# Optimization experiments

Measured on AMD Instinct MI355X. Metric: run time of the kernel, lower is better.

## Reference

```python
import jax, jax.numpy as jnp
import numpy as np

N_NODES = 100000
N_EDGES = 1600000
IN_DIM = 128
HID = 128
OUT = 112


def setup_inputs() -> dict:
    key = jax.random.key(0)
    ks = jax.random.split(key, 8)
    s = 1.0 / np.sqrt(IN_DIM)
    sh = 1.0 / np.sqrt(HID)
    return {
        "x": jax.random.normal(ks[0], (N_NODES, IN_DIM), jnp.float32),
        "edge_index": jax.random.randint(ks[1], (2, N_EDGES), 0, N_NODES, jnp.int64),
        "W_l1": jax.random.normal(ks[2], (HID, IN_DIM), jnp.float32) * s,
        "b_l1": jnp.zeros((HID,), jnp.float32),
        "W_r1": jax.random.normal(ks[3], (HID, IN_DIM), jnp.float32) * s,
        "W_l2": jax.random.normal(ks[4], (HID, HID), jnp.float32) * sh,
        "b_l2": jnp.zeros((HID,), jnp.float32),
        "W_r2": jax.random.normal(ks[5], (HID, HID), jnp.float32) * sh,
        "W_out": jax.random.normal(ks[6], (OUT, HID), jnp.float32) * sh,
        "b_out": jnp.zeros((OUT,), jnp.float32),
    }


def _sage_conv(x, edge_index, W_l, b_l, W_r):
    # PyG SAGEConv, aggr='mean', root_weight=True:
    #   out_i = W_l @ mean_{j in N(i)} x_j + b_l + W_r @ x_i
    src, dst = edge_index[0], edge_index[1]
    n = x.shape[0]
    agg = jax.ops.segment_sum(x[src], dst, num_segments=n)          # [N, d]
    deg = jax.ops.segment_sum(jnp.ones_like(dst, dtype=x.dtype), dst, num_segments=n)
    mean = agg / jnp.maximum(deg, 1.0)[:, None]
    return mean @ W_l.T + b_l + x @ W_r.T


def reference(x, edge_index, W_l1, b_l1, W_r1, W_l2, b_l2, W_r2, W_out, b_out):
    h = jax.nn.relu(_sage_conv(x, edge_index, W_l1, b_l1, W_r1))
    # dropout p=0.2 is identity at inference (training=False)
    h = jax.nn.relu(_sage_conv(h, edge_index, W_l2, b_l2, W_r2))
    return h @ W_out.T + b_out  # [N, 112] logits
```

## Files before the change

### kernel.cpp

```cpp
#include <hip/hip_runtime.h>
#include <hip/hip_bf16.h>

#define HID 128
#define OUT_DIM 112
#define CAP 4096

typedef short bf16x8 __attribute__((ext_vector_type(8)));
typedef float f32x4 __attribute__((ext_vector_type(4)));

__device__ __forceinline__ ushort f2b(float f) {
  __hip_bfloat16 h = __float2bfloat16(f);
  return *reinterpret_cast<ushort*>(&h);
}

__global__ __launch_bounds__(256) void f2b_kernel(
    const float* __restrict__ in, ushort* __restrict__ out, int n4) {
  int i = blockIdx.x * 256 + threadIdx.x;
  if (i >= n4) return;
  float4 v = ((const float4*)in)[i];
  ushort4 r;
  r.x = f2b(v.x); r.y = f2b(v.y); r.z = f2b(v.z); r.w = f2b(v.w);
  ((ushort4*)out)[i] = r;
}

__global__ __launch_bounds__(256) void packw_kernel(
    const float* __restrict__ W, ushort* __restrict__ wb, int ntiles, int total) {
  int p = blockIdx.x * 256 + threadIdx.x;
  if (p >= total) return;
  int j = p & 7;
  int l = (p >> 3) & 63;
  int rest = p >> 9;
  int nt = rest % ntiles;
  int ks = rest / ntiles;
  int nn = nt * 16 + (l & 15);
  int k = ks * 32 + (l >> 4) * 8 + j;
  wb[p] = f2b(W[nn * 128 + k]);
}

__global__ __launch_bounds__(256) void hist_kernel(
    const int* __restrict__ dst, int* __restrict__ gcount, int e, int nb) {
  __shared__ int lh[1024];
  const int t = threadIdx.x;
  for (int i = t; i < nb; i += 256) lh[i] = 0;
  __syncthreads();
  int base = blockIdx.x * 4096;
#pragma unroll
  for (int j = 0; j < 16; ++j) {
    int i = base + j * 256 + t;
    if (i < e) atomicAdd(&lh[dst[i] >> 7], 1);
  }
  __syncthreads();
  for (int i = t; i < nb; i += 256)
    if (lh[i]) atomicAdd(&gcount[i], lh[i]);
}

__global__ __launch_bounds__(1024) void scan_nb_kernel(
    const int* __restrict__ gcount, int* __restrict__ gbase,
    int* __restrict__ gcursor, int* __restrict__ rowstart,
    int e, int n, int nb) {
  __shared__ int wsum[16];
  const int t = threadIdx.x, lane = t & 63, wid = t >> 6;
  int v = (t < nb) ? gcount[t] : 0;
  int s = v;
#pragma unroll
  for (int off = 1; off < 64; off <<= 1) {
    int u = __shfl_up(s, off, 64);
    if (lane >= off) s += u;
  }
  if (lane == 63) wsum[wid] = s;
  __syncthreads();
  if (wid == 0) {
    int ws = (lane < 16) ? wsum[lane] : 0;
#pragma unroll
    for (int off = 1; off < 16; off <<= 1) {
      int u = __shfl_up(ws, off, 64);
      if (lane >= off) ws += u;
    }
    if (lane < 16) wsum[lane] = ws;
  }
  __syncthreads();
  int excl = s - v + (wid ? wsum[wid - 1] : 0);
  if (t < nb) {
    gbase[t] = excl;
    gcursor[t] = excl;
  }
  if (t == 0) {
    gbase[nb] = e;
    rowstart[n] = e;
  }
}

__global__ __launch_bounds__(1024) void bucket_scatter_kernel(
    const int* __restrict__ src, const int* __restrict__ dst,
    int* __restrict__ gcursor, uint* __restrict__ bedges, int e, int nb) {
  __shared__ int lh[1024];
  __shared__ int lstart[1024];
  __shared__ int wsum[16];
  __shared__ uint sp[8192];
  __shared__ ushort sb[8192];
  const int t = threadIdx.x, lane = t & 63, wid = t >> 6;
  const int base = blockIdx.x * 8192;
  const int ecnt = min(8192, e - base);
  for (int i = t; i < nb; i += 1024) lh[i] = 0;
  __syncthreads();
  int myb[8], myr[8];
  uint myp[8];
#pragma unroll
  for (int j = 0; j < 8; ++j) {
    int i = base + j * 1024 + t;
    myb[j] = -1;
    if (i < e) {
      int d = dst[i];
      int sv = src[i];
      int b = d >> 7;
      myb[j] = b;
      myp[j] = ((uint)sv << 7) | (uint)(d & 127);
      myr[j] = atomicAdd(&lh[b], 1);
    }
  }
  __syncthreads();
  int cnt = (t < nb) ? lh[t] : 0;
  int s = cnt;
#pragma unroll
  for (int off = 1; off < 64; off <<= 1) {
    int u = __shfl_up(s, off, 64);
    if (lane >= off) s += u;
  }
  if (lane == 63) wsum[wid] = s;
  __syncthreads();
  if (wid == 0) {
    int ws = (lane < 16) ? wsum[lane] : 0;
#pragma unroll
    for (int off = 1; off < 16; off <<= 1) {
      int u = __shfl_up(ws, off, 64);
      if (lane >= off) ws += u;
    }
    if (lane < 16) wsum[lane] = ws;
  }
  __syncthreads();
  int excl = s - cnt + (wid ? wsum[wid - 1] : 0);
  if (t < nb) lstart[t] = excl;
  __syncthreads();
  if (t < nb) lh[t] = (cnt > 0) ? atomicAdd(&gcursor[t], cnt) : 0;
  __syncthreads();
#pragma unroll
  for (int j = 0; j < 8; ++j) {
    if (myb[j] >= 0) {
      int slot = lstart[myb[j]] + myr[j];
      sp[slot] = myp[j];
      sb[slot] = (ushort)myb[j];
    }
  }
  __syncthreads();
#pragma unroll
  for (int j = 0; j < 8; ++j) {
    int i = j * 1024 + t;
    if (i < ecnt) {
      int b = sb[i];
      int pos = lh[b] + (i - lstart[b]);
      bedges[pos] = sp[i];
    }
  }
}

__global__ __launch_bounds__(256) void csr_build_kernel(
    const uint* __restrict__ bedges, const int* __restrict__ gbase,
    int* __restrict__ rowstart, float* __restrict__ dinv,
    int* __restrict__ csr_src, int n) {
  __shared__ int lh[128];
  __shared__ int lst[128];
  __shared__ int lcur[128];
  __shared__ int wsum2[4];
  __shared__ int lsorted[CAP];
  const int t = threadIdx.x;
  const int bkt = blockIdx.x;
  const int node0 = bkt << 7;
  const int g0 = gbase[bkt], g1 = gbase[bkt + 1];
  const int cnt = g1 - g0;
  if (t < 128) lh[t] = 0;
  __syncthreads();
  for (int i = t; i < cnt; i += 256)
    atomicAdd(&lh[bedges[g0 + i] & 127], 1);
  __syncthreads();
  const int lane = t & 63, wid = t >> 6;
  int v = (t < 128) ? lh[t] : 0;
  int s = v;
#pragma unroll
  for (int off = 1; off < 64; off <<= 1) {
    int u = __shfl_up(s, off, 64);
    if (lane >= off) s += u;
  }
  if (t < 128 && lane == 63) wsum2[wid] = s;
  __syncthreads();
  int excl = s - v + ((wid == 1) ? wsum2[0] : 0);
  if (t < 128) {
    lst[t] = excl;
    lcur[t] = excl;
    int node = node0 + t;
    if (node < n) {
      rowstart[node] = g0 + excl;
      dinv[node] = 1.0f / (float)max(v, 1);
    }
  }
  __syncthreads();
  for (int i = t; i < cnt; i += 256) {
    uint p = bedges[g0 + i];
    int d = p & 127;
    int slot = atomicAdd(&lcur[d], 1);
    int sv = (int)(p >> 7);
    if (slot < CAP) lsorted[slot] = sv;
    else csr_src[g0 + slot] = sv;
  }
  __syncthreads();
  int lim = min(cnt, CAP);
  for (int i = t; i < lim; i += 256) csr_src[g0 + i] = lsorted[i];
}

__global__ __launch_bounds__(256) void agg_bf16_kernel(
    const ushort* __restrict__ xb, const int* __restrict__ csr_src,
    const int* __restrict__ rowstart, const float* __restrict__ dinv,
    ushort* __restrict__ aggb, int n) {
  int node = blockIdx.x * 4 + (threadIdx.x >> 6);
  int lane = threadIdx.x & 63;
  if (node >= n) return;
  int s = rowstart[node], e1 = rowstart[node + 1];
  float ax = 0.f, ay = 0.f;
  int e = s;
  for (; e + 4 <= e1; e += 4) {
    int s0 = csr_src[e], s1 = csr_src[e + 1], s2 = csr_src[e + 2], s3 = csr_src[e + 3];
    uint u0 = ((const uint*)(xb + (size_t)s0 * 128))[lane];
    uint u1 = ((const uint*)(xb + (size_t)s1 * 128))[lane];
    uint u2 = ((const uint*)(xb + (size_t)s2 * 128))[lane];
    uint u3 = ((const uint*)(xb + (size_t)s3 * 128))[lane];
    ax += (__uint_as_float(u0 << 16) + __uint_as_float(u1 << 16)) +
          (__uint_as_float(u2 << 16) + __uint_as_float(u3 << 16));
    ay += (__uint_as_float(u0 & 0xffff0000u) + __uint_as_float(u1 & 0xffff0000u)) +
          (__uint_as_float(u2 & 0xffff0000u) + __uint_as_float(u3 & 0xffff0000u));
  }
  for (; e < e1; ++e) {
    uint u = ((const uint*)(xb + (size_t)csr_src[e] * 128))[lane];
    ax += __uint_as_float(u << 16);
    ay += __uint_as_float(u & 0xffff0000u);
  }
  float sc = dinv[node];
  uint r = (uint)f2b(ax * sc) | ((uint)f2b(ay * sc) << 16);
  ((uint*)(aggb + (size_t)node * 128))[lane] = r;
}

__global__ __launch_bounds__(256) void lin_mfma_kernel(
    const ushort* __restrict__ meanb, const ushort* __restrict__ xb,
    const ushort* __restrict__ wb, const float* __restrict__ bias,
    ushort* __restrict__ outb, int n) {
  __shared__ ushort zA[64 * 128];
  __shared__ ushort zX[64 * 128];
  const int t = threadIdx.x;
  const int block0 = blockIdx.x * 64;
#pragma unroll
  for (int i = 0; i < 4; ++i) {
    int c = i * 256 + t;
    int row = c >> 4;
    int col = c & 15;
    int node = block0 + row;
    int4 va = make_int4(0, 0, 0, 0), vx = make_int4(0, 0, 0, 0);
    if (node < n) {
      va = ((const int4*)(meanb + (size_t)node * 128))[col];
      vx = ((const int4*)(xb + (size_t)node * 128))[col];
    }
    ((int4*)zA)[c] = va;
    ((int4*)zX)[c] = vx;
  }
  __syncthreads();
  const int lane = t & 63;
  const int wave = t >> 6;
  const int m0 = wave * 16;
  const int cidx = lane & 15;
  const int quad = lane >> 4;
  f32x4 acc[8];
#pragma unroll
  for (int nt = 0; nt < 8; ++nt) acc[nt] = (f32x4){0.f, 0.f, 0.f, 0.f};
#pragma unroll
  for (int s = 0; s < 2; ++s) {
    const ushort* zs = (s == 0) ? zA : zX;
#pragma unroll
    for (int ks = 0; ks < 4; ++ks) {
      bf16x8 a = *(const bf16x8*)(zs + (m0 + cidx) * 128 + ks * 32 + quad * 8);
      const ushort* wp = wb + ((size_t)((s * 4 + ks) * 8) * 64 + lane) * 8;
#pragma unroll
      for (int nt = 0; nt < 8; ++nt) {
        bf16x8 b = *(const bf16x8*)(wp + nt * 512);
        acc[nt] = __builtin_amdgcn_mfma_f32_16x16x32_bf16(a, b, acc[nt], 0, 0, 0);
      }
    }
  }
  __syncthreads();
#pragma unroll
  for (int nt = 0; nt < 8; ++nt) {
    float bv = bias[nt * 16 + cidx];
#pragma unroll
    for (int i = 0; i < 4; ++i) {
      float v = fmaxf(acc[nt][i] + bv, 0.f);
      zA[(m0 + quad * 4 + i) * 128 + nt * 16 + cidx] = f2b(v);
    }
  }
  __syncthreads();
#pragma unroll
  for (int i = 0; i < 4; ++i) {
    int c = i * 256 + t;
    int row = c >> 4;
    int col = c & 15;
    int node = block0 + row;
    if (node < n) ((int4*)(outb + (size_t)node * 128))[col] = ((const int4*)zA)[c];
  }
}

__global__ __launch_bounds__(256) void out_mfma_kernel(
    const ushort* __restrict__ h2b, const ushort* __restrict__ wb,
    const float* __restrict__ bias, float* __restrict__ outp, int n) {
  __shared__ ushort zt[64 * 128];
  __shared__ float zo[64 * 112];
  const int t = threadIdx.x;
  const int block0 = blockIdx.x * 64;
#pragma unroll
  for (int i = 0; i < 4; ++i) {
    int c = i * 256 + t;
    int row = c >> 4;
    int col = c & 15;
    int node = block0 + row;
    int4 v = make_int4(0, 0, 0, 0);
    if (node < n) v = ((const int4*)(h2b + (size_t)node * 128))[col];
    ((int4*)zt)[c] = v;
  }
  __syncthreads();
  const int lane = t & 63;
  const int wave = t >> 6;
  const int m0 = wave * 16;
  const int cidx = lane & 15;
  const int quad = lane >> 4;
  f32x4 acc[7];
#pragma unroll
  for (int nt = 0; nt < 7; ++nt) acc[nt] = (f32x4){0.f, 0.f, 0.f, 0.f};
#pragma unroll
  for (int ks = 0; ks < 4; ++ks) {
    bf16x8 a = *(const bf16x8*)(zt + (m0 + cidx) * 128 + ks * 32 + quad * 8);
    const ushort* wp = wb + ((size_t)(ks * 7) * 64 + lane) * 8;
#pragma unroll
    for (int nt = 0; nt < 7; ++nt) {
      bf16x8 b = *(const bf16x8*)(wp + nt * 512);
      acc[nt] = __builtin_amdgcn_mfma_f32_16x16x32_bf16(a, b, acc[nt], 0, 0, 0);
    }
  }
#pragma unroll
  for (int nt = 0; nt < 7; ++nt) {
    float bv = bias[nt * 16 + cidx];
#pragma unroll
    for (int i = 0; i < 4; ++i)
      zo[(m0 + quad * 4 + i) * 112 + nt * 16 + cidx] = acc[nt][i] + bv;
  }
  __syncthreads();
#pragma unroll
  for (int i = 0; i < 7; ++i) {
    int c = i * 256 + t;
    int node = block0 + c / 28;
    if (node < n)
      ((float4*)(outp + (size_t)block0 * 112))[c] = ((const float4*)zo)[c];
  }
}

extern "C" void kernel_launch(void* const* d_in, const int* in_sizes, int n_in,
                              void* d_out, int out_size, void* d_ws, size_t ws_size,
                              hipStream_t stream) {
  const float* x     = (const float*)d_in[0];
  const int*   ei    = (const int*)d_in[1];
  const float* W_l1  = (const float*)d_in[2];
  const float* b_l1  = (const float*)d_in[3];
  const float* W_r1  = (const float*)d_in[4];
  const float* W_l2  = (const float*)d_in[5];
  const float* b_l2  = (const float*)d_in[6];
  const float* W_r2  = (const float*)d_in[7];
  const float* W_out = (const float*)d_in[8];
  const float* b_out = (const float*)d_in[9];

  const int N = in_sizes[0] / 128;
  const int E = in_sizes[1] / 2;
  const int NB = (N + 127) >> 7;
  const int* src = ei;
  const int* dst = ei + E;

  ushort* XB = (ushort*)d_ws;
  ushort* MB = XB + (size_t)N * 128;
  ushort* HB = MB + (size_t)N * 128;
  float* DINV = (float*)(HB + (size_t)N * 128);
  ushort* WB1 = (ushort*)(DINV + N);
  ushort* WB2 = WB1 + 32768;
  ushort* WBO = WB2 + 32768;
  int* GCOUNT   = (int*)(WBO + 14336);
  int* GBASE    = GCOUNT + NB;
  int* GCURSOR  = GBASE + NB + 1;
  int* ROWSTART = GCURSOR + NB;
  uint* BEDGES  = (uint*)(ROWSTART + N + 1);
  int* CSRSRC   = (int*)(BEDGES + E);

  hipMemsetAsync(GCOUNT, 0, (size_t)NB * sizeof(int), stream);
  hist_kernel<<<(E + 4095) / 4096, 256, 0, stream>>>(dst, GCOUNT, E, NB);
  scan_nb_kernel<<<1, 1024, 0, stream>>>(GCOUNT, GBASE, GCURSOR, ROWSTART, E, N, NB);
  bucket_scatter_kernel<<<(E + 8191) / 8192, 1024, 0, stream>>>(
      src, dst, GCURSOR, BEDGES, E, NB);
  csr_build_kernel<<<NB, 256, 0, stream>>>(BEDGES, GBASE, ROWSTART, DINV, CSRSRC, N);

  int n4 = N * 128 / 4;
  f2b_kernel<<<(n4 + 255) / 256, 256, 0, stream>>>(x, XB, n4);
  packw_kernel<<<64, 256, 0, stream>>>(W_l1, WB1, 8, 16384);
  packw_kernel<<<64, 256, 0, stream>>>(W_r1, WB1 + 16384, 8, 16384);
  packw_kernel<<<64, 256, 0, stream>>>(W_l2, WB2, 8, 16384);
  packw_kernel<<<64, 256, 0, stream>>>(W_r2, WB2 + 16384, 8, 16384);
  packw_kernel<<<56, 256, 0, stream>>>(W_out, WBO, 7, 14336);

  int ablocks = (N + 3) / 4;
  int lblocks = (N + 63) / 64;

  agg_bf16_kernel<<<ablocks, 256, 0, stream>>>(XB, CSRSRC, ROWSTART, DINV, MB, N);
  lin_mfma_kernel<<<lblocks, 256, 0, stream>>>(MB, XB, WB1, b_l1, HB, N);

  agg_bf16_kernel<<<ablocks, 256, 0, stream>>>(HB, CSRSRC, ROWSTART, DINV, MB, N);
  lin_mfma_kernel<<<lblocks, 256, 0, stream>>>(MB, HB, WB2, b_l2, XB, N);

  out_mfma_kernel<<<lblocks, 256, 0, stream>>>(XB, WBO, b_out, (float*)d_out, N);
}
```

Measured before the change: 375.5 us.

## Fuse neighbor aggregation into SAGE linear kernels and fold output layer

```diff
diff --git a/kernel.cpp b/kernel.cpp
--- a/kernel.cpp
+++ b/kernel.cpp
@@ -23,18 +23,29 @@
   ((ushort4*)out)[i] = r;
 }
 
-__global__ __launch_bounds__(256) void packw_kernel(
-    const float* __restrict__ W, ushort* __restrict__ wb, int ntiles, int total) {
+__global__ __launch_bounds__(256) void packw_all_kernel(
+    const float* __restrict__ Wl1, const float* __restrict__ Wr1,
+    const float* __restrict__ Wl2, const float* __restrict__ Wr2,
+    const float* __restrict__ Wo, ushort* __restrict__ WB1,
+    ushort* __restrict__ WB2, ushort* __restrict__ WBO) {
   int p = blockIdx.x * 256 + threadIdx.x;
-  if (p >= total) return;
-  int j = p & 7;
-  int l = (p >> 3) & 63;
-  int rest = p >> 9;
+  const float* W;
+  ushort* wb;
+  int ntiles, off;
+  if (p < 16384)      { W = Wl1; wb = WB1;         ntiles = 8; off = p; }
+  else if (p < 32768) { W = Wr1; wb = WB1 + 16384; ntiles = 8; off = p - 16384; }
+  else if (p < 49152) { W = Wl2; wb = WB2;         ntiles = 8; off = p - 32768; }
+  else if (p < 65536) { W = Wr2; wb = WB2 + 16384; ntiles = 8; off = p - 49152; }
+  else if (p < 79872) { W = Wo;  wb = WBO;         ntiles = 7; off = p - 65536; }
+  else return;
+  int j = off & 7;
+  int l = (off >> 3) & 63;
+  int rest = off >> 9;
   int nt = rest % ntiles;
   int ks = rest / ntiles;
   int nn = nt * 16 + (l & 15);
   int k = ks * 32 + (l >> 4) * 8 + j;
-  wb[p] = f2b(W[nn * 128 + k]);
+  wb[off] = f2b(W[nn * 128 + k]);
 }
 
 __global__ __launch_bounds__(256) void hist_kernel(
@@ -216,62 +227,66 @@
   for (int i = t; i < lim; i += 256) csr_src[g0 + i] = lsorted[i];
 }
 
-__global__ __launch_bounds__(256) void agg_bf16_kernel(
+__device__ __forceinline__ void gather_tile(
     const ushort* __restrict__ xb, const int* __restrict__ csr_src,
     const int* __restrict__ rowstart, const float* __restrict__ dinv,
-    ushort* __restrict__ aggb, int n) {
-  int node = blockIdx.x * 4 + (threadIdx.x >> 6);
-  int lane = threadIdx.x & 63;
-  if (node >= n) return;
-  int s = rowstart[node], e1 = rowstart[node + 1];
-  float ax = 0.f, ay = 0.f;
-  int e = s;
-  for (; e + 4 <= e1; e += 4) {
-    int s0 = csr_src[e], s1 = csr_src[e + 1], s2 = csr_src[e + 2], s3 = csr_src[e + 3];
-    uint u0 = ((const uint*)(xb + (size_t)s0 * 128))[lane];
-    uint u1 = ((const uint*)(xb + (size_t)s1 * 128))[lane];
-    uint u2 = ((const uint*)(xb + (size_t)s2 * 128))[lane];
-    uint u3 = ((const uint*)(xb + (size_t)s3 * 128))[lane];
-    ax += (__uint_as_float(u0 << 16) + __uint_as_float(u1 << 16)) +
-          (__uint_as_float(u2 << 16) + __uint_as_float(u3 << 16));
-    ay += (__uint_as_float(u0 & 0xffff0000u) + __uint_as_float(u1 & 0xffff0000u)) +
-          (__uint_as_float(u2 & 0xffff0000u) + __uint_as_float(u3 & 0xffff0000u));
-  }
-  for (; e < e1; ++e) {
-    uint u = ((const uint*)(xb + (size_t)csr_src[e] * 128))[lane];
-    ax += __uint_as_float(u << 16);
-    ay += __uint_as_float(u & 0xffff0000u);
-  }
-  float sc = dinv[node];
-  uint r = (uint)f2b(ax * sc) | ((uint)f2b(ay * sc) << 16);
-  ((uint*)(aggb + (size_t)node * 128))[lane] = r;
-}
-
-__global__ __launch_bounds__(256) void lin_mfma_kernel(
-    const ushort* __restrict__ meanb, const ushort* __restrict__ xb,
+    ushort* __restrict__ zA, int block0, int n, int wave, int lane) {
+#pragma unroll 1
+  for (int j = 0; j < 16; ++j) {
+    int lrow = wave * 16 + j;
+    int node = block0 + lrow;
+    uint r = 0;
+    if (node < n) {
+      int s = rowstart[node], e1 = rowstart[node + 1];
+      float ax = 0.f, ay = 0.f;
+      int e = s;
+      for (; e + 4 <= e1; e += 4) {
+        int s0 = csr_src[e], s1 = csr_src[e + 1];
+        int s2 = csr_src[e + 2], s3 = csr_src[e + 3];
+        uint u0 = ((const uint*)(xb + (size_t)s0 * 128))[lane];
+        uint u1 = ((const uint*)(xb + (size_t)s1 * 128))[lane];
+        uint u2 = ((const uint*)(xb + (size_t)s2 * 128))[lane];
+        uint u3 = ((const uint*)(xb + (size_t)s3 * 128))[lane];
+        ax += (__uint_as_float(u0 << 16) + __uint_as_float(u1 << 16)) +
+              (__uint_as_float(u2 << 16) + __uint_as_float(u3 << 16));
+        ay += (__uint_as_float(u0 & 0xffff0000u) + __uint_as_float(u1 & 0xffff0000u)) +
+              (__uint_as_float(u2 & 0xffff0000u) + __uint_as_float(u3 & 0xffff0000u));
+      }
+      for (; e < e1; ++e) {
+        uint u = ((const uint*)(xb + (size_t)csr_src[e] * 128))[lane];
+        ax += __uint_as_float(u << 16);
+        ay += __uint_as_float(u & 0xffff0000u);
+      }
+      float sc = dinv[node];
+      r = (uint)f2b(ax * sc) | ((uint)f2b(ay * sc) << 16);
+    }
+    ((uint*)(zA + lrow * 128))[lane] = r;
+  }
+}
+
+__global__ __launch_bounds__(256) void sage1_kernel(
+    const ushort* __restrict__ xb, const int* __restrict__ csr_src,
+    const int* __restrict__ rowstart, const float* __restrict__ dinv,
     const ushort* __restrict__ wb, const float* __restrict__ bias,
     ushort* __restrict__ outb, int n) {
   __shared__ ushort zA[64 * 128];
   __shared__ ushort zX[64 * 128];
   const int t = threadIdx.x;
   const int block0 = blockIdx.x * 64;
+  const int lane = t & 63;
+  const int wave = t >> 6;
 #pragma unroll
   for (int i = 0; i < 4; ++i) {
     int c = i * 256 + t;
     int row = c >> 4;
     int col = c & 15;
     int node = block0 + row;
-    int4 va = make_int4(0, 0, 0, 0), vx = make_int4(0, 0, 0, 0);
-    if (node < n) {
-      va = ((const int4*)(meanb + (size_t)node * 128))[col];
-      vx = ((const int4*)(xb + (size_t)node * 128))[col];
-    }
-    ((int4*)zA)[c] = va;
+    int4 vx = make_int4(0, 0, 0, 0);
+    if (node < n) vx = ((const int4*)(xb + (size_t)node * 128))[col];
     ((int4*)zX)[c] = vx;
   }
-  __syncthreads();
-  const int lane = t & 63;
-  const int wave = t >> 6;
+  gather_tile(xb, csr_src, rowstart, dinv, zA, block0, n, wave, lane);
+  __syncthreads();
   const int m0 = wave * 16;
   const int cidx = lane & 15;
   const int quad = lane >> 4;
@@ -313,56 +328,81 @@
   }
 }
 
-__global__ __launch_bounds__(256) void out_mfma_kernel(
-    const ushort* __restrict__ h2b, const ushort* __restrict__ wb,
-    const float* __restrict__ bias, float* __restrict__ outp, int n) {
-  __shared__ ushort zt[64 * 128];
-  __shared__ float zo[64 * 112];
+__global__ __launch_bounds__(256) void sage2_kernel(
+    const ushort* __restrict__ hb, const int* __restrict__ csr_src,
+    const int* __restrict__ rowstart, const float* __restrict__ dinv,
+    const ushort* __restrict__ wb, const float* __restrict__ bias,
+    const ushort* __restrict__ wbo, const float* __restrict__ bias_o,
+    float* __restrict__ outp, int n) {
+  __shared__ ushort zA[64 * 128];
+  __shared__ ushort zX[64 * 128];
   const int t = threadIdx.x;
   const int block0 = blockIdx.x * 64;
+  const int lane = t & 63;
+  const int wave = t >> 6;
 #pragma unroll
   for (int i = 0; i < 4; ++i) {
     int c = i * 256 + t;
     int row = c >> 4;
     int col = c & 15;
     int node = block0 + row;
-    int4 v = make_int4(0, 0, 0, 0);
-    if (node < n) v = ((const int4*)(h2b + (size_t)node * 128))[col];
-    ((int4*)zt)[c] = v;
-  }
-  __syncthreads();
-  const int lane = t & 63;
-  const int wave = t >> 6;
+    int4 vx = make_int4(0, 0, 0, 0);
+    if (node < n) vx = ((const int4*)(hb + (size_t)node * 128))[col];
+    ((int4*)zX)[c] = vx;
+  }
+  gather_tile(hb, csr_src, rowstart, dinv, zA, block0, n, wave, lane);
+  __syncthreads();
   const int m0 = wave * 16;
   const int cidx = lane & 15;
   const int quad = lane >> 4;
-  f32x4 acc[7];
-#pragma unroll
-  for (int nt = 0; nt < 7; ++nt) acc[nt] = (f32x4){0.f, 0.f, 0.f, 0.f};
+  f32x4 acc[8];
+#pragma unroll
+  for (int nt = 0; nt < 8; ++nt) acc[nt] = (f32x4){0.f, 0.f, 0.f, 0.f};
+#pragma unroll
+  for (int s = 0; s < 2; ++s) {
+    const ushort* zs = (s == 0) ? zA : zX;
+#pragma unroll
+    for (int ks = 0; ks < 4; ++ks) {
+      bf16x8 a = *(const bf16x8*)(zs + (m0 + cidx) * 128 + ks * 32 + quad * 8);
+      const ushort* wp = wb + ((size_t)((s * 4 + ks) * 8) * 64 + lane) * 8;
+#pragma unroll
+      for (int nt = 0; nt < 8; ++nt) {
+        bf16x8 b = *(const bf16x8*)(wp + nt * 512);
+        acc[nt] = __builtin_amdgcn_mfma_f32_16x16x32_bf16(a, b, acc[nt], 0, 0, 0);
+      }
+    }
+  }
+#pragma unroll
+  for (int nt = 0; nt < 8; ++nt) {
+    float bv = bias[nt * 16 + cidx];
+#pragma unroll
+    for (int i = 0; i < 4; ++i) {
+      float v = fmaxf(acc[nt][i] + bv, 0.f);
+      zX[(m0 + quad * 4 + i) * 128 + nt * 16 + cidx] = f2b(v);
+    }
+  }
+  f32x4 acc2[7];
+#pragma unroll
+  for (int nt = 0; nt < 7; ++nt) acc2[nt] = (f32x4){0.f, 0.f, 0.f, 0.f};
 #pragma unroll
   for (int ks = 0; ks < 4; ++ks) {
-    bf16x8 a = *(const bf16x8*)(zt + (m0 + cidx) * 128 + ks * 32 + quad * 8);
-    const ushort* wp = wb + ((size_t)(ks * 7) * 64 + lane) * 8;
+    bf16x8 a = *(const bf16x8*)(zX + (m0 + cidx) * 128 + ks * 32 + quad * 8);
+    const ushort* wp = wbo + ((size_t)(ks * 7) * 64 + lane) * 8;
 #pragma unroll
     for (int nt = 0; nt < 7; ++nt) {
       bf16x8 b = *(const bf16x8*)(wp + nt * 512);
-      acc[nt] = __builtin_amdgcn_mfma_f32_16x16x32_bf16(a, b, acc[nt], 0, 0, 0);
+      acc2[nt] = __builtin_amdgcn_mfma_f32_16x16x32_bf16(a, b, acc2[nt], 0, 0, 0);
     }
   }
 #pragma unroll
   for (int nt = 0; nt < 7; ++nt) {
-    float bv = bias[nt * 16 + cidx];
-#pragma unroll
-    for (int i = 0; i < 4; ++i)
-      zo[(m0 + quad * 4 + i) * 112 + nt * 16 + cidx] = acc[nt][i] + bv;
-  }
-  __syncthreads();
-#pragma unroll
-  for (int i = 0; i < 7; ++i) {
-    int c = i * 256 + t;
-    int node = block0 + c / 28;
-    if (node < n)
-      ((float4*)(outp + (size_t)block0 * 112))[c] = ((const float4*)zo)[c];
+    float bv = bias_o[nt * 16 + cidx];
+#pragma unroll
+    for (int i = 0; i < 4; ++i) {
+      int node = block0 + m0 + quad * 4 + i;
+      if (node < n)
+        outp[(size_t)node * OUT_DIM + nt * 16 + cidx] = acc2[nt][i] + bv;
+    }
   }
 }
 
@@ -387,8 +427,7 @@
   const int* dst = ei + E;
 
   ushort* XB = (ushort*)d_ws;
-  ushort* MB = XB + (size_t)N * 128;
-  ushort* HB = MB + (size_t)N * 128;
+  ushort* HB = XB + (size_t)N * 128;
   float* DINV = (float*)(HB + (size_t)N * 128);
   ushort* WB1 = (ushort*)(DINV + N);
   ushort* WB2 = WB1 + 32768;
@@ -409,20 +448,13 @@
 
   int n4 = N * 128 / 4;
   f2b_kernel<<<(n4 + 255) / 256, 256, 0, stream>>>(x, XB, n4);
-  packw_kernel<<<64, 256, 0, stream>>>(W_l1, WB1, 8, 16384);
-  packw_kernel<<<64, 256, 0, stream>>>(W_r1, WB1 + 16384, 8, 16384);
-  packw_kernel<<<64, 256, 0, stream>>>(W_l2, WB2, 8, 16384);
-  packw_kernel<<<64, 256, 0, stream>>>(W_r2, WB2 + 16384, 8, 16384);
-  packw_kernel<<<56, 256, 0, stream>>>(W_out, WBO, 7, 14336);
-
-  int ablocks = (N + 3) / 4;
+  packw_all_kernel<<<312, 256, 0, stream>>>(W_l1, W_r1, W_l2, W_r2, W_out,
+                                            WB1, WB2, WBO);
+
   int lblocks = (N + 63) / 64;
-
-  agg_bf16_kernel<<<ablocks, 256, 0, stream>>>(XB, CSRSRC, ROWSTART, DINV, MB, N);
-  lin_mfma_kernel<<<lblocks, 256, 0, stream>>>(MB, XB, WB1, b_l1, HB, N);
-
-  agg_bf16_kernel<<<ablocks, 256, 0, stream>>>(HB, CSRSRC, ROWSTART, DINV, MB, N);
-  lin_mfma_kernel<<<lblocks, 256, 0, stream>>>(MB, HB, WB2, b_l2, XB, N);
-
-  out_mfma_kernel<<<lblocks, 256, 0, stream>>>(XB, WBO, b_out, (float*)d_out, N);
-}
+  sage1_kernel<<<lblocks, 256, 0, stream>>>(XB, CSRSRC, ROWSTART, DINV,
+                                            WB1, b_l1, HB, N);
+  sage2_kernel<<<lblocks, 256, 0, stream>>>(HB, CSRSRC, ROWSTART, DINV,
+                                            WB2, b_l2, WBO, b_out,
+                                            (float*)d_out, N);
+}
```

After: 464.5 us. +23.7%, slower.
